# Optimization experiments

Hardware: AMD Instinct MI355X
Metric: run time of the kernel (lower is better)

The kernel has to match this reference:

```python
import jax, jax.numpy as jnp
import numpy as np
from jax import lax


def _conv2d(x, w, b, stride):
    # x: [B,C,H,W], w: [O,I,kh,kw], b: [O]
    y = lax.conv_general_dilated(
        x, w, window_strides=(stride, stride), padding='VALID',
        dimension_numbers=('NCHW', 'OIHW', 'NCHW'))
    return y + b[None, :, None, None]


def setup_inputs() -> dict:
    key = jax.random.key(0)
    ks = jax.random.split(key, 4)
    B, C, H, W = 8, 128, 128, 128
    x = jax.random.normal(ks[0], (B, C, H, W), dtype=jnp.float32)
    # conv weights, scaled like torch default init (~1/sqrt(fan_in))
    Wq = jax.random.normal(ks[1], (C, C, 2, 2), dtype=jnp.float32) / np.sqrt(C * 4)
    Wk = jax.random.normal(ks[2], (C, C, 2, 2), dtype=jnp.float32) / np.sqrt(C * 4)
    Wv = jax.random.normal(ks[3], (C, C, 1, 1), dtype=jnp.float32) / np.sqrt(C)
    bq = jnp.zeros((C,), dtype=jnp.float32)
    bk = jnp.zeros((C,), dtype=jnp.float32)
    bv = jnp.zeros((C,), dtype=jnp.float32)
    return {'x': x, 'Wq': Wq, 'bq': bq, 'Wk': Wk, 'bk': bk, 'Wv': Wv, 'bv': bv}


def reference(x, Wq, bq, Wk, bk, Wv, bv):
    B, C, H, W = x.shape
    # query/key: 2x2 stride-2 convs -> [B, C, (H//2)*(W//2)]
    q = _conv2d(x, Wq, bq, 2).reshape(B, C, -1)
    k = _conv2d(x, Wk, bk, 2).reshape(B, C, -1)
    # value: 1x1 conv -> [B, C, H*W]
    v = _conv2d(x, Wv, bv, 1).reshape(B, C, -1)
    # energy: [B, C, C]
    energy = jnp.einsum('bcn,bdn->bcd', q, k)
    # max-subtract trick: softmax over (row_max - energy)
    energy_new = jnp.max(energy, axis=-1, keepdims=True) - energy
    attention = jax.nn.softmax(energy_new, axis=-1)
    out = jnp.einsum('bcd,bdn->bcn', attention, v)
    return out.reshape(B, C, H, W)
```

## Files before the change

kernel.cpp:

```cpp
#include <hip/hip_runtime.h>
#include <math.h>


typedef float f32x4 __attribute__((ext_vector_type(4)));
typedef short s16x8 __attribute__((ext_vector_type(8)));

__device__ __forceinline__ unsigned short f2bf(float f) {
  union { float f; unsigned u; } v; v.f = f;
  unsigned r = v.u + 0x7FFFu + ((v.u >> 16) & 1u);
  return (unsigned short)(r >> 16);
}
__device__ __forceinline__ float bf2f(unsigned short h) {
  union { unsigned u; float f; } v; v.u = ((unsigned)h) << 16;
  return v.f;
}
__device__ __forceinline__ unsigned pack2(unsigned short a, unsigned short b) {
  return (unsigned)a | ((unsigned)b << 16);
}

__device__ __forceinline__ void stage_pair(unsigned short* Bh, unsigned short* Bl,
                                           int nl, int kloc, float4 v) {
  unsigned short hx = f2bf(v.x), hy = f2bf(v.y), hz = f2bf(v.z), hw = f2bf(v.w);
  unsigned short lx = f2bf(v.x - bf2f(hx)), ly = f2bf(v.y - bf2f(hy));
  unsigned short lz = f2bf(v.z - bf2f(hz)), lw = f2bf(v.w - bf2f(hw));
  *(unsigned*)&Bh[nl * 40 + kloc]       = pack2(hx, hy);
  *(unsigned*)&Bh[(nl + 1) * 40 + kloc] = pack2(hz, hw);
  *(unsigned*)&Bl[nl * 40 + kloc]       = pack2(lx, ly);
  *(unsigned*)&Bl[(nl + 1) * 40 + kloc] = pack2(lz, lw);
}

__global__ __launch_bounds__(256) void k_prep(
    const float* __restrict__ Wq, const float* __restrict__ Wk,
    unsigned short* __restrict__ Wth, unsigned short* __restrict__ Wtl) {
  const int f = (blockIdx.x * 256 + threadIdx.x) * 4;
  const int row = f >> 9;
  const int k   = f & 511;
  const float* src = (row < 128) ? &Wq[row * 512 + k] : &Wk[(row - 128) * 512 + k];
  float4 v = *(const float4*)src;
  unsigned short h0 = f2bf(v.x), h1 = f2bf(v.y), h2 = f2bf(v.z), h3 = f2bf(v.w);
  unsigned short l0 = f2bf(v.x - bf2f(h0)), l1 = f2bf(v.y - bf2f(h1));
  unsigned short l2 = f2bf(v.z - bf2f(h2)), l3 = f2bf(v.w - bf2f(h3));
  const int di = (k >> 5) * 8192 + row * 32 + (k & 31);
  *(ushort4*)&Wth[di] = make_ushort4(h0, h1, h2, h3);
  *(ushort4*)&Wtl[di] = make_ushort4(l0, l1, l2, l3);
}

__global__ __launch_bounds__(256, 2) void k_conv_energy(
    const float* __restrict__ x,
    const unsigned short* __restrict__ Wth, const unsigned short* __restrict__ Wtl,
    const float* __restrict__ bq, const float* __restrict__ bk,
    float* __restrict__ epart) {
  __shared__ unsigned short LDS[32768];
  unsigned short* Th = LDS;
  unsigned short* Tl = LDS + 16384;

  const int t = threadIdx.x;
  const int nt = blockIdx.x, b = blockIdx.y;
  const int w = t >> 6, lane = t & 63;
  const int lrow = lane & 15, lkb = lane >> 4;

  const int pp = t >> 4;
  const int ci_l = pp >> 1, kh = pp & 1;
  const int c0 = (t & 15) * 8;
  const int klb = ci_l * 4 + kh * 2;
  const float* xb = x + ((size_t)b << 21);
  const float* xrow = xb + (size_t)ci_l * 16384 + (2 * nt + kh) * 128 + c0;

  f32x4 acc[4][4];
#pragma unroll
  for (int m = 0; m < 4; ++m)
#pragma unroll
    for (int n = 0; n < 4; ++n) acc[m][n] = (f32x4){0.f, 0.f, 0.f, 0.f};

  {
    float4 v1 = *(const float4*)&xrow[0];
    float4 v2 = *(const float4*)&xrow[4];
    stage_pair(LDS, LDS + 2560, c0 >> 1, klb, v1);
    stage_pair(LDS, LDS + 2560, (c0 >> 1) + 2, klb, v2);
  }
  __syncthreads();

  int cur = 0;
  for (int step = 0; step < 16; ++step) {
    float4 pv1, pv2;
    if (step < 15) {
      const float* xr = xrow + (size_t)(step + 1) * 8 * 16384;
      pv1 = *(const float4*)&xr[0];
      pv2 = *(const float4*)&xr[4];
    }
    s16x8 afh[4], afl[4], bfh[4], bfl[4];
    {
      const unsigned short* Wh_s = Wth + step * 8192;
      const unsigned short* Wl_s = Wtl + step * 8192;
#pragma unroll
      for (int m = 0; m < 4; ++m) {
        const int off = (w * 64 + m * 16 + lrow) * 32 + lkb * 8;
        afh[m] = *(const s16x8*)&Wh_s[off];
        afl[m] = *(const s16x8*)&Wl_s[off];
      }
    }
    const unsigned short* Bh = LDS + cur * 5120;
    const unsigned short* Bl = Bh + 2560;
#pragma unroll
    for (int nf = 0; nf < 4; ++nf) {
      const int bidx = (nf * 16 + lrow) * 40 + lkb * 8;
      bfh[nf] = *(const s16x8*)&Bh[bidx];
      bfl[nf] = *(const s16x8*)&Bl[bidx];
    }
#pragma unroll
    for (int m = 0; m < 4; ++m)
#pragma unroll
      for (int n = 0; n < 4; ++n) {
        acc[m][n] = __builtin_amdgcn_mfma_f32_16x16x32_bf16(afh[m], bfh[n], acc[m][n], 0, 0, 0);
        acc[m][n] = __builtin_amdgcn_mfma_f32_16x16x32_bf16(afh[m], bfl[n], acc[m][n], 0, 0, 0);
        acc[m][n] = __builtin_amdgcn_mfma_f32_16x16x32_bf16(afl[m], bfh[n], acc[m][n], 0, 0, 0);
      }
    if (step < 15) {
      unsigned short* Nh = LDS + (cur ^ 1) * 5120;
      unsigned short* Nl = Nh + 2560;
      stage_pair(Nh, Nl, c0 >> 1, klb, pv1);
      stage_pair(Nh, Nl, (c0 >> 1) + 2, klb, pv2);
    }
    __syncthreads();
    cur ^= 1;
  }

  const float* biasp = (w < 2) ? bq : bk;
  const int rb = (w & 1) * 64;
  float biasr[16];
#pragma unroll
  for (int m = 0; m < 4; ++m)
#pragma unroll
    for (int i = 0; i < 4; ++i)
      biasr[m * 4 + i] = biasp[rb + m * 16 + (lane >> 4) * 4 + i];

#pragma unroll
  for (int m = 0; m < 4; ++m) {
    const int r0 = w * 64 + m * 16 + (lane >> 4) * 4;
#pragma unroll
    for (int n = 0; n < 4; ++n) {
      const int c = n * 16 + lrow;
      const int c8 = c >> 3, c7 = c & 7;
#pragma unroll
      for (int i = 0; i < 4; ++i) {
        const int r = r0 + i;
        const float vv = acc[m][n][i] + biasr[m * 4 + i];
        const unsigned short h = f2bf(vv);
        const unsigned short l = f2bf(vv - bf2f(h));
        const int ad = r * 64 + (((c8 ^ (r & 7))) << 3) + c7;
        Th[ad] = h;
        Tl[ad] = l;
      }
    }
  }
  __syncthreads();

  f32x4 e[4][4];
#pragma unroll
  for (int m = 0; m < 4; ++m)
#pragma unroll
    for (int n = 0; n < 4; ++n) e[m][n] = (f32x4){0.f, 0.f, 0.f, 0.f};

  const int mrow0 = (w >> 1) * 64;
  const int nrow0 = 128 + (w & 1) * 64;
#pragma unroll
  for (int ks = 0; ks < 2; ++ks) {
    const int c8 = ks * 4 + lkb;
    s16x8 qh[4], ql[4], kh8[4], kl8[4];
#pragma unroll
    for (int m = 0; m < 4; ++m) {
      const int r = mrow0 + m * 16 + lrow;
      const int ad = r * 64 + ((c8 ^ (r & 7)) << 3);
      qh[m] = *(const s16x8*)&Th[ad];
      ql[m] = *(const s16x8*)&Tl[ad];
    }
#pragma unroll
    for (int n = 0; n < 4; ++n) {
      const int r = nrow0 + n * 16 + lrow;
      const int ad = r * 64 + ((c8 ^ (r & 7)) << 3);
      kh8[n] = *(const s16x8*)&Th[ad];
      kl8[n] = *(const s16x8*)&Tl[ad];
    }
#pragma unroll
    for (int m = 0; m < 4; ++m)
#pragma unroll
      for (int n = 0; n < 4; ++n) {
        e[m][n] = __builtin_amdgcn_mfma_f32_16x16x32_bf16(qh[m], kh8[n], e[m][n], 0, 0, 0);
        e[m][n] = __builtin_amdgcn_mfma_f32_16x16x32_bf16(qh[m], kl8[n], e[m][n], 0, 0, 0);
        e[m][n] = __builtin_amdgcn_mfma_f32_16x16x32_bf16(ql[m], kh8[n], e[m][n], 0, 0, 0);
      }
  }
  float* ep = epart + ((size_t)b * 64 + nt) * 16384;
#pragma unroll
  for (int m = 0; m < 4; ++m) {
    const int qr = (w >> 1) * 64 + m * 16 + (lane >> 4) * 4;
#pragma unroll
    for (int n = 0; n < 4; ++n) {
      const int kr = (w & 1) * 64 + n * 16 + lrow;
#pragma unroll
      for (int i = 0; i < 4; ++i) ep[(size_t)(qr + i) * 128 + kr] = e[m][n][i];
    }
  }
}

__global__ __launch_bounds__(256) void k_softmax_M(
    const float* __restrict__ epart, const float* __restrict__ Wv,
    const float* __restrict__ bv, float* __restrict__ Mbuf,
    float* __restrict__ outbb) {
  __shared__ float As[4][128];
  const int t = threadIdx.x;
  const int wid = t >> 6, lane = t & 63;
  const int b = blockIdx.x >> 5;
  const int c = (blockIdx.x & 31) * 4 + wid;
  const int d0 = lane * 2;

  float2 s = make_float2(0.f, 0.f);
#pragma unroll 4
  for (int p = 0; p < 64; ++p) {
    float2 e = *(const float2*)&epart[((size_t)b * 64 + p) * 16384 + c * 128 + d0];
    s.x += e.x; s.y += e.y;
  }
  float mn = fminf(s.x, s.y);
#pragma unroll
  for (int off = 1; off < 64; off <<= 1) mn = fminf(mn, __shfl_xor(mn, off));
  const float p0 = expf(mn - s.x);
  const float p1 = expf(mn - s.y);
  float tot = p0 + p1;
#pragma unroll
  for (int off = 1; off < 64; off <<= 1) tot += __shfl_xor(tot, off);
  const float inv = 1.f / tot;
  const float a0 = p0 * inv, a1 = p1 * inv;

  const float2 bvv = *(const float2*)&bv[d0];
  float ob = a0 * bvv.x + a1 * bvv.y;
#pragma unroll
  for (int off = 1; off < 64; off <<= 1) ob += __shfl_xor(ob, off);
  if (lane == 0) outbb[b * 128 + c] = ob;

  As[wid][d0] = a0;
  As[wid][d0 + 1] = a1;
  float m0 = 0.f, m1 = 0.f;
#pragma unroll 4
  for (int d = 0; d < 128; ++d) {
    const float a = As[wid][d];
    const float2 wv = *(const float2*)&Wv[d * 128 + d0];
    m0 = fmaf(a, wv.x, m0);
    m1 = fmaf(a, wv.y, m1);
  }
  *(float2*)&Mbuf[(size_t)b * 16384 + c * 128 + d0] = make_float2(m0, m1);
}

__global__ __launch_bounds__(256) void k_out(
    const float* __restrict__ x, const float* __restrict__ Mbuf,
    const float* __restrict__ outbb, float* __restrict__ out) {
  __shared__ unsigned short Ms[128 * 40];
  __shared__ unsigned short Xs[128 * 40];
  const int t = threadIdx.x;
  const int nt = blockIdx.x, b = blockIdx.y;
  const int wid = t >> 6, lane = t & 63;
  const int wr = wid >> 1, wc = wid & 1;
  const int lrow = lane & 15, lkb = lane >> 4;
  const int am = t >> 1, ak0 = (t & 1) * 16;
  const int xkl = (t >> 5) * 4;
  const int xc0 = (t & 31) * 4;

  const float* xb = x + ((size_t)b << 21);
  const float* Mb = Mbuf + (size_t)b * 16384;
  float* ob = out + ((size_t)b << 21);

  f32x4 acc[4][4];
#pragma unroll
  for (int m = 0; m < 4; ++m)
#pragma unroll
    for (int n = 0; n < 4; ++n) acc[m][n] = (f32x4){0.f, 0.f, 0.f, 0.f};

  for (int step = 0; step < 4; ++step) {
    const int kk = step * 32;
    {
      float w[16];
      *(float4*)&w[0]  = *(const float4*)&Mb[am * 128 + kk + ak0];
      *(float4*)&w[4]  = *(const float4*)&Mb[am * 128 + kk + ak0 + 4];
      *(float4*)&w[8]  = *(const float4*)&Mb[am * 128 + kk + ak0 + 8];
      *(float4*)&w[12] = *(const float4*)&Mb[am * 128 + kk + ak0 + 12];
      unsigned short hs[16];
#pragma unroll
      for (int i = 0; i < 16; ++i) hs[i] = f2bf(w[i]);
      *(uint4*)&Ms[am * 40 + ak0]     = *(uint4*)&hs[0];
      *(uint4*)&Ms[am * 40 + ak0 + 8] = *(uint4*)&hs[8];
    }
#pragma unroll
    for (int q = 0; q < 4; ++q) {
      const int kl = xkl + q;
      float4 v = *(const float4*)&xb[(size_t)(kk + kl) * 16384 + nt * 128 + xc0];
      Xs[(xc0 + 0) * 40 + kl] = f2bf(v.x);
      Xs[(xc0 + 1) * 40 + kl] = f2bf(v.y);
      Xs[(xc0 + 2) * 40 + kl] = f2bf(v.z);
      Xs[(xc0 + 3) * 40 + kl] = f2bf(v.w);
    }
    __syncthreads();
    s16x8 af[4], bf[4];
#pragma unroll
    for (int m = 0; m < 4; ++m)
      af[m] = *(const s16x8*)&Ms[(wr * 64 + m * 16 + lrow) * 40 + lkb * 8];
#pragma unroll
    for (int n = 0; n < 4; ++n)
      bf[n] = *(const s16x8*)&Xs[(wc * 64 + n * 16 + lrow) * 40 + lkb * 8];
#pragma unroll
    for (int m = 0; m < 4; ++m)
#pragma unroll
      for (int n = 0; n < 4; ++n)
        acc[m][n] = __builtin_amdgcn_mfma_f32_16x16x32_bf16(af[m], bf[n], acc[m][n], 0, 0, 0);
    __syncthreads();
  }
#pragma unroll
  for (int m = 0; m < 4; ++m) {
    const int r0 = wr * 64 + m * 16 + (lane >> 4) * 4;
#pragma unroll
    for (int n = 0; n < 4; ++n) {
      const int gc = nt * 128 + wc * 64 + n * 16 + (lane & 15);
#pragma unroll
      for (int i = 0; i < 4; ++i) {
        const int row = r0 + i;
        ob[(size_t)row * 16384 + gc] = acc[m][n][i] + outbb[b * 128 + row];
      }
    }
  }
}

extern "C" void kernel_launch(void* const* d_in, const int* in_sizes, int n_in,
                              void* d_out, int out_size, void* d_ws, size_t ws_size,
                              hipStream_t stream) {
  const float* x  = (const float*)d_in[0];
  const float* Wq = (const float*)d_in[1];
  const float* bq = (const float*)d_in[2];
  const float* Wk = (const float*)d_in[3];
  const float* bk = (const float*)d_in[4];
  const float* Wv = (const float*)d_in[5];
  const float* bv = (const float*)d_in[6];
  float* out = (float*)d_out;
  char* ws = (char*)d_ws;

  float* epart = (float*)ws;
  float* Mbuf  = (float*)(ws + 33554432);
  float* outbb = (float*)(ws + 34078720);
  unsigned short* Wth = (unsigned short*)(ws + 34082816);
  unsigned short* Wtl = (unsigned short*)(ws + 34344960);

  hipLaunchKernelGGL(k_prep, dim3(128), dim3(256), 0, stream, Wq, Wk, Wth, Wtl);
  hipLaunchKernelGGL(k_conv_energy, dim3(64, 8), dim3(256), 0, stream,
                     x, Wth, Wtl, bq, bk, epart);
  hipLaunchKernelGGL(k_softmax_M, dim3(256), dim3(256), 0, stream,
                     epart, Wv, bv, Mbuf, outbb);
  hipLaunchKernelGGL(k_out, dim3(128, 8), dim3(256), 0, stream,
                     x, Mbuf, outbb, out);
}
```

Before: 87.62 us.

## Prefetch weight fragments one step ahead and remap x staging to avoid LDS conflicts

Measured after the change: 87.01 us. Within noise of the previous version (-0.7%).

```diff
diff --git a/kernel.cpp b/kernel.cpp
--- a/kernel.cpp
+++ b/kernel.cpp
@@ -16,17 +16,6 @@
 }
 __device__ __forceinline__ unsigned pack2(unsigned short a, unsigned short b) {
   return (unsigned)a | ((unsigned)b << 16);
-}
-
-__device__ __forceinline__ void stage_pair(unsigned short* Bh, unsigned short* Bl,
-                                           int nl, int kloc, float4 v) {
-  unsigned short hx = f2bf(v.x), hy = f2bf(v.y), hz = f2bf(v.z), hw = f2bf(v.w);
-  unsigned short lx = f2bf(v.x - bf2f(hx)), ly = f2bf(v.y - bf2f(hy));
-  unsigned short lz = f2bf(v.z - bf2f(hz)), lw = f2bf(v.w - bf2f(hw));
-  *(unsigned*)&Bh[nl * 40 + kloc]       = pack2(hx, hy);
-  *(unsigned*)&Bh[(nl + 1) * 40 + kloc] = pack2(hz, hw);
-  *(unsigned*)&Bl[nl * 40 + kloc]       = pack2(lx, ly);
-  *(unsigned*)&Bl[(nl + 1) * 40 + kloc] = pack2(lz, lw);
 }
 
 __global__ __launch_bounds__(256) void k_prep(
@@ -61,10 +50,10 @@
 
   const int pp = t >> 4;
   const int ci_l = pp >> 1, kh = pp & 1;
-  const int c0 = (t & 15) * 8;
+  const int i16 = t & 15;
   const int klb = ci_l * 4 + kh * 2;
   const float* xb = x + ((size_t)b << 21);
-  const float* xrow = xb + (size_t)ci_l * 16384 + (2 * nt + kh) * 128 + c0;
+  const float* xrow = xb + (size_t)ci_l * 16384 + (2 * nt + kh) * 128 + 2 * i16;
 
   f32x4 acc[4][4];
 #pragma unroll
@@ -72,35 +61,50 @@
 #pragma unroll
     for (int n = 0; n < 4; ++n) acc[m][n] = (f32x4){0.f, 0.f, 0.f, 0.f};
 
+  s16x8 pfh[2][4], pfl[2][4];
+  const int aoff = (w * 64 + lrow) * 32 + lkb * 8;
+
+#pragma unroll
+  for (int m = 0; m < 4; ++m) {
+    pfh[0][m] = *(const s16x8*)&Wth[aoff + m * 512];
+    pfl[0][m] = *(const s16x8*)&Wtl[aoff + m * 512];
+  }
   {
-    float4 v1 = *(const float4*)&xrow[0];
-    float4 v2 = *(const float4*)&xrow[4];
-    stage_pair(LDS, LDS + 2560, c0 >> 1, klb, v1);
-    stage_pair(LDS, LDS + 2560, (c0 >> 1) + 2, klb, v2);
+#pragma unroll
+    for (int g = 0; g < 4; ++g) {
+      const int n = i16 + 16 * g;
+      float2 v = *(const float2*)&xrow[32 * g];
+      unsigned short hx = f2bf(v.x), hy = f2bf(v.y);
+      *(unsigned*)&LDS[n * 40 + klb]        = pack2(hx, hy);
+      *(unsigned*)&LDS[2560 + n * 40 + klb] = pack2(f2bf(v.x - bf2f(hx)),
+                                                    f2bf(v.y - bf2f(hy)));
+    }
   }
   __syncthreads();
 
-  int cur = 0;
+#pragma unroll
   for (int step = 0; step < 16; ++step) {
-    float4 pv1, pv2;
+    const int cb = step & 1;
+    if (step < 15) {
+      const unsigned short* Wh_n = Wth + (step + 1) * 8192;
+      const unsigned short* Wl_n = Wtl + (step + 1) * 8192;
+#pragma unroll
+      for (int m = 0; m < 4; ++m) {
+        pfh[cb ^ 1][m] = *(const s16x8*)&Wh_n[aoff + m * 512];
+        pfl[cb ^ 1][m] = *(const s16x8*)&Wl_n[aoff + m * 512];
+      }
+    }
+    float2 pv0, pv1, pv2, pv3;
     if (step < 15) {
       const float* xr = xrow + (size_t)(step + 1) * 8 * 16384;
-      pv1 = *(const float4*)&xr[0];
-      pv2 = *(const float4*)&xr[4];
-    }
-    s16x8 afh[4], afl[4], bfh[4], bfl[4];
-    {
-      const unsigned short* Wh_s = Wth + step * 8192;
-      const unsigned short* Wl_s = Wtl + step * 8192;
-#pragma unroll
-      for (int m = 0; m < 4; ++m) {
-        const int off = (w * 64 + m * 16 + lrow) * 32 + lkb * 8;
-        afh[m] = *(const s16x8*)&Wh_s[off];
-        afl[m] = *(const s16x8*)&Wl_s[off];
-      }
-    }
-    const unsigned short* Bh = LDS + cur * 5120;
+      pv0 = *(const float2*)&xr[0];
+      pv1 = *(const float2*)&xr[32];
+      pv2 = *(const float2*)&xr[64];
+      pv3 = *(const float2*)&xr[96];
+    }
+    const unsigned short* Bh = LDS + cb * 5120;
     const unsigned short* Bl = Bh + 2560;
+    s16x8 bfh[4], bfl[4];
 #pragma unroll
     for (int nf = 0; nf < 4; ++nf) {
       const int bidx = (nf * 16 + lrow) * 40 + lkb * 8;
@@ -111,18 +115,39 @@
     for (int m = 0; m < 4; ++m)
 #pragma unroll
       for (int n = 0; n < 4; ++n) {
-        acc[m][n] = __builtin_amdgcn_mfma_f32_16x16x32_bf16(afh[m], bfh[n], acc[m][n], 0, 0, 0);
-        acc[m][n] = __builtin_amdgcn_mfma_f32_16x16x32_bf16(afh[m], bfl[n], acc[m][n], 0, 0, 0);
-        acc[m][n] = __builtin_amdgcn_mfma_f32_16x16x32_bf16(afl[m], bfh[n], acc[m][n], 0, 0, 0);
+        acc[m][n] = __builtin_amdgcn_mfma_f32_16x16x32_bf16(pfh[cb][m], bfh[n], acc[m][n], 0, 0, 0);
+        acc[m][n] = __builtin_amdgcn_mfma_f32_16x16x32_bf16(pfh[cb][m], bfl[n], acc[m][n], 0, 0, 0);
+        acc[m][n] = __builtin_amdgcn_mfma_f32_16x16x32_bf16(pfl[cb][m], bfh[n], acc[m][n], 0, 0, 0);
       }
     if (step < 15) {
-      unsigned short* Nh = LDS + (cur ^ 1) * 5120;
+      unsigned short* Nh = LDS + (cb ^ 1) * 5120;
       unsigned short* Nl = Nh + 2560;
-      stage_pair(Nh, Nl, c0 >> 1, klb, pv1);
-      stage_pair(Nh, Nl, (c0 >> 1) + 2, klb, pv2);
+      {
+        const int n = i16;
+        unsigned short hx = f2bf(pv0.x), hy = f2bf(pv0.y);
+        *(unsigned*)&Nh[n * 40 + klb] = pack2(hx, hy);
+        *(unsigned*)&Nl[n * 40 + klb] = pack2(f2bf(pv0.x - bf2f(hx)), f2bf(pv0.y - bf2f(hy)));
+      }
+      {
+        const int n = i16 + 16;
+        unsigned short hx = f2bf(pv1.x), hy = f2bf(pv1.y);
+        *(unsigned*)&Nh[n * 40 + klb] = pack2(hx, hy);
+        *(unsigned*)&Nl[n * 40 + klb] = pack2(f2bf(pv1.x - bf2f(hx)), f2bf(pv1.y - bf2f(hy)));
+      }
+      {
+        const int n = i16 + 32;
+        unsigned short hx = f2bf(pv2.x), hy = f2bf(pv2.y);
+        *(unsigned*)&Nh[n * 40 + klb] = pack2(hx, hy);
+        *(unsigned*)&Nl[n * 40 + klb] = pack2(f2bf(pv2.x - bf2f(hx)), f2bf(pv2.y - bf2f(hy)));
+      }
+      {
+        const int n = i16 + 48;
+        unsigned short hx = f2bf(pv3.x), hy = f2bf(pv3.y);
+        *(unsigned*)&Nh[n * 40 + klb] = pack2(hx, hy);
+        *(unsigned*)&Nl[n * 40 + klb] = pack2(f2bf(pv3.x - bf2f(hx)), f2bf(pv3.y - bf2f(hy)));
+      }
     }
     __syncthreads();
-    cur ^= 1;
   }
 
   const float* biasp = (w < 2) ? bq : bk;
```
